# Kernel tuning notes

Measured on AMD Instinct MI355X. Metric: run time of the kernel, lower is better.

Reference implementation:

```python
import jax, jax.numpy as jnp
import numpy as np

DIM = 512
H = 8
HD = DIM // H
B = 1
S = 4096
SCALE = HD ** -0.5


def setup_inputs() -> dict:
    key = jax.random.key(0)
    k1, k2, k3, k4, k5 = jax.random.split(key, 5)
    bound = DIM ** -0.5
    x = jax.random.normal(k1, (B, S, DIM), dtype=jnp.float32)
    q_param = jax.random.uniform(k2, (DIM, H, HD), dtype=jnp.float32, minval=-bound, maxval=bound)
    k_param = jax.random.uniform(k3, (DIM, H, HD), dtype=jnp.float32, minval=-bound, maxval=bound)
    v_param = jax.random.uniform(k4, (DIM, H, HD), dtype=jnp.float32, minval=-bound, maxval=bound)
    p_param = jax.random.uniform(k5, (H, HD, DIM), dtype=jnp.float32, minval=-bound, maxval=bound)
    return {"x": x, "q_param": q_param, "k_param": k_param, "v_param": v_param, "p_param": p_param}


def reference(x, q_param, k_param, v_param, p_param):
    q = jnp.einsum('bsc,chd->bshd', x, q_param) * SCALE
    k = jnp.einsum('btc,chd->bthd', x, k_param)
    v = jnp.einsum('btc,chd->bthd', x, v_param)
    attn = jax.nn.softmax(jnp.einsum('bshd,bthd->bhst', q, k), axis=-1)  # [B,H,S,S]
    o = jnp.einsum('bhst,bthd->bshd', attn, v)
    return jnp.einsum('bshd,hdc->bsc', o, p_param)
```

## Files before the change

kernel.cpp:

```cpp
#include <hip/hip_runtime.h>
#include <hip/hip_bf16.h>
#include <stdint.h>

#define S_LEN 4096
#define DIM   512
#define NH    8
#define HD    64
#define QSCALE 0.18033688011112042f

typedef __attribute__((ext_vector_type(8))) short short8;
typedef __attribute__((ext_vector_type(4))) float f32x4;
typedef __attribute__((ext_vector_type(16))) float f32x16;
typedef __attribute__((ext_vector_type(2))) unsigned uint2v;

__device__ __forceinline__ uint32_t pk2(float lo, float hi) {
  union { __hip_bfloat162 h; uint32_t u; } cv;
  cv.h = __float22bfloat162_rn(float2{lo, hi});
  return cv.u;
}
__device__ __forceinline__ ushort bf1(float x) {
  union { __hip_bfloat16 b; ushort u; } cv;
  cv.b = __float2bfloat16(x);
  return cv.u;
}
__device__ __forceinline__ float bf2f(ushort u) {
  union { uint32_t u; float f; } cv;
  cv.u = (uint32_t)u << 16;
  return cv.f;
}
__device__ __forceinline__ float fexp2(float x) {
  float r;
  asm("v_exp_f32 %0, %1" : "=v"(r) : "v"(x));
  return r;
}

__global__ __launch_bounds__(256)
void cast_x(const float* __restrict__ src, ushort* __restrict__ dst) {
  const int i = (blockIdx.x * 256 + threadIdx.x) * 8;
  const float4 a = *reinterpret_cast<const float4*>(src + i);
  const float4 b = *reinterpret_cast<const float4*>(src + i + 4);
  uint4 o;
  o.x = pk2(a.x, a.y); o.y = pk2(a.z, a.w);
  o.z = pk2(b.x, b.y); o.w = pk2(b.z, b.w);
  *reinterpret_cast<uint4*>(dst + i) = o;
}

__global__ __launch_bounds__(256)
void transpose_w(const float* __restrict__ qp, const float* __restrict__ kp,
                 const float* __restrict__ vp, const float* __restrict__ pp,
                 ushort* __restrict__ wbT, ushort* __restrict__ ppT) {
  __shared__ float L[64][65];
  const int z = blockIdx.z;
  const float* src = (z == 0) ? qp : (z == 1) ? kp : (z == 2) ? vp : pp;
  ushort* dst = (z < 3) ? (wbT + (size_t)z * 512 * 512) : ppT;
  const float scale = (z == 0) ? QSCALE : 1.0f;
  const int k0 = blockIdx.x * 64, n0 = blockIdx.y * 64;
  const int r = threadIdx.x >> 2, c0 = (threadIdx.x & 3) * 16;

#pragma unroll
  for (int j = 0; j < 4; ++j) {
    const float4 v =
        *reinterpret_cast<const float4*>(&src[(k0 + r) * 512 + n0 + c0 + 4 * j]);
    L[r][c0 + 4 * j + 0] = v.x * scale;
    L[r][c0 + 4 * j + 1] = v.y * scale;
    L[r][c0 + 4 * j + 2] = v.z * scale;
    L[r][c0 + 4 * j + 3] = v.w * scale;
  }
  __syncthreads();

  uint4 u0, u1;
  u0.x = pk2(L[c0 + 0][r], L[c0 + 1][r]);
  u0.y = pk2(L[c0 + 2][r], L[c0 + 3][r]);
  u0.z = pk2(L[c0 + 4][r], L[c0 + 5][r]);
  u0.w = pk2(L[c0 + 6][r], L[c0 + 7][r]);
  u1.x = pk2(L[c0 + 8][r], L[c0 + 9][r]);
  u1.y = pk2(L[c0 + 10][r], L[c0 + 11][r]);
  u1.z = pk2(L[c0 + 12][r], L[c0 + 13][r]);
  u1.w = pk2(L[c0 + 14][r], L[c0 + 15][r]);
  ushort* d = dst + (size_t)(n0 + r) * 512 + k0 + c0;
  *reinterpret_cast<uint4*>(d) = u0;
  *reinterpret_cast<uint4*>(d + 8) = u1;
}

template <int MODE>
__global__ __launch_bounds__(256)
void gemm_bf16(const ushort* __restrict__ A, const ushort* __restrict__ Bt,
               void* __restrict__ Cout) {
  __shared__ __align__(16) unsigned char lds[24576];
  const int tid = threadIdx.x;
  const int m0 = blockIdx.x * 128, n0 = blockIdx.y * 64;
  const int lane = tid & 63, w = tid >> 6;
  const int wm = w >> 1, wn = w & 1;
  const int q = lane & 15, g = lane >> 4;
  f32x4 acc[4][2] = {};

  const int ar = tid >> 1, ah = tid & 1;
  const int br = tid >> 2, bq = tid & 3;

  for (int k0 = 0; k0 < 512; k0 += 64) {
    const ushort* ag = A + (size_t)(m0 + ar) * 512 + k0 + ah * 32;
    const uint4 a0 = *reinterpret_cast<const uint4*>(ag);
    const uint4 a1 = *reinterpret_cast<const uint4*>(ag + 8);
    const uint4 a2 = *reinterpret_cast<const uint4*>(ag + 16);
    const uint4 a3 = *reinterpret_cast<const uint4*>(ag + 24);
    const ushort* bg = Bt + (size_t)(n0 + br) * 512 + k0 + bq * 16;
    const uint4 b0 = *reinterpret_cast<const uint4*>(bg);
    const uint4 b1 = *reinterpret_cast<const uint4*>(bg + 8);
    __syncthreads();
    {
      unsigned char* ab = lds + ar * 128;
      const int asw = (ar & 7) << 4;
      *reinterpret_cast<uint4*>(ab + ((ah * 64 + 0) ^ asw)) = a0;
      *reinterpret_cast<uint4*>(ab + ((ah * 64 + 16) ^ asw)) = a1;
      *reinterpret_cast<uint4*>(ab + ((ah * 64 + 32) ^ asw)) = a2;
      *reinterpret_cast<uint4*>(ab + ((ah * 64 + 48) ^ asw)) = a3;
      unsigned char* bb = lds + 16384 + br * 128;
      const int bsw = (br & 7) << 4;
      *reinterpret_cast<uint4*>(bb + ((bq * 32 + 0) ^ bsw)) = b0;
      *reinterpret_cast<uint4*>(bb + ((bq * 32 + 16) ^ bsw)) = b1;
    }
    __syncthreads();

#pragma unroll
    for (int ks = 0; ks < 2; ++ks) {
      short8 bf[2];
#pragma unroll
      for (int ni = 0; ni < 2; ++ni) {
        const int rn = wn * 32 + ni * 16 + q;
        bf[ni] = *reinterpret_cast<const short8*>(
            lds + 16384 + rn * 128 + ((64 * ks + 16 * g) ^ ((rn & 7) << 4)));
      }
#pragma unroll
      for (int mi = 0; mi < 4; ++mi) {
        const int rm = wm * 64 + mi * 16 + q;
        const short8 af = *reinterpret_cast<const short8*>(
            lds + rm * 128 + ((64 * ks + 16 * g) ^ ((rm & 7) << 4)));
#pragma unroll
        for (int ni = 0; ni < 2; ++ni)
          acc[mi][ni] = __builtin_amdgcn_mfma_f32_16x16x32_bf16(
              af, bf[ni], acc[mi][ni], 0, 0, 0);
      }
    }
  }

  if (MODE == 0) {
    ushort* C = (ushort*)Cout;
    const int which = n0 >> 9;
#pragma unroll
    for (int ni = 0; ni < 2; ++ni) {
      const int n = n0 + wn * 32 + ni * 16 + q;
      const int rem = n & 511, hh = rem >> 6, d = rem & 63;
      if (which == 2) {
        ushort* base = C + (size_t)(2 * NH + hh) * (size_t)(S_LEN * HD) +
                       (size_t)d * S_LEN;
#pragma unroll
        for (int mi = 0; mi < 4; ++mi) {
          const int s = m0 + wm * 64 + mi * 16 + 4 * g;
          uint2 pw;
          pw.x = pk2(acc[mi][ni][0], acc[mi][ni][1]);
          pw.y = pk2(acc[mi][ni][2], acc[mi][ni][3]);
          *reinterpret_cast<uint2*>(base + s) = pw;
        }
      } else {
        ushort* base =
            C + ((size_t)which * NH + hh) * (size_t)(S_LEN * HD) + d;
#pragma unroll
        for (int mi = 0; mi < 4; ++mi) {
          const int s = m0 + wm * 64 + mi * 16 + 4 * g;
#pragma unroll
          for (int r = 0; r < 4; ++r)
            base[(size_t)(s + r) * HD] = bf1(acc[mi][ni][r]);
        }
      }
    }
  } else {
    float* C = (float*)Cout;
#pragma unroll
    for (int ni = 0; ni < 2; ++ni) {
      const int n = n0 + wn * 32 + ni * 16 + q;
#pragma unroll
      for (int mi = 0; mi < 4; ++mi) {
        const int s = m0 + wm * 64 + mi * 16 + 4 * g;
#pragma unroll
        for (int r = 0; r < 4; ++r)
          C[(size_t)(s + r) * 512 + n] = acc[mi][ni][r];
      }
    }
  }
}

__global__ __launch_bounds__(256, 4)
void attn_mfma32(const ushort* __restrict__ QKV, ushort* __restrict__ Opart,
                 float2* __restrict__ ML) {
  __shared__ __align__(16) unsigned char lds[32768];
  const int tid = threadIdx.x;
  const int combo = blockIdx.x;
  const int h = combo & 7, z = combo >> 3;
  const int qb = blockIdx.y;
  const int lane = tid & 63, w = tid >> 6;
  const int r31 = lane & 31, hh = lane >> 5;

  const size_t plane = (size_t)S_LEN * HD;
  const ushort* Qp = QKV + (size_t)h * plane;
  const ushort* Kp = QKV + (size_t)(NH + h) * plane;
  const ushort* Vp = QKV + (size_t)(2 * NH + h) * plane;

  const int qrow = qb * 128 + w * 32 + r31;

  short8 qf[4];
  {
    const ushort* qptr = Qp + (size_t)qrow * HD + 8 * hh;
#pragma unroll
    for (int ks = 0; ks < 4; ++ks)
      qf[ks] = *reinterpret_cast<const short8*>(qptr + 16 * ks);
  }

  int raddr[4];
#pragma unroll
  for (int ks = 0; ks < 4; ++ks)
    raddr[ks] = r31 * 128 + (((2 * ks + hh) ^ (r31 & 7)) << 4);

  const int trow = tid >> 2, seg = tid & 3;
  const int swr = (trow & 7) << 4;
  const int wk0 = trow * 128 + ((seg * 32) ^ swr);
  const int wk1 = trow * 128 + ((seg * 32 + 16) ^ swr);
  const ushort* kgbase = Kp + (size_t)(z * 1024 + trow) * HD + seg * 16;
  const ushort* vgbase = Vp + (size_t)trow * S_LEN + z * 1024 + seg * 16;

  f32x16 o[2] = {};
  float m_i = -1e30f, l_i = 0.f;

  uint4 kA = *reinterpret_cast<const uint4*>(kgbase);
  uint4 kB = *reinterpret_cast<const uint4*>(kgbase + 8);
  uint4 vA = *reinterpret_cast<const uint4*>(vgbase);
  uint4 vB = *reinterpret_cast<const uint4*>(vgbase + 8);

  for (int t = 0; t < 16; ++t) {
    const int po = (t & 1) << 14;
    *reinterpret_cast<uint4*>(lds + (wk0 | po)) = kA;
    *reinterpret_cast<uint4*>(lds + (wk1 | po)) = kB;
    *reinterpret_cast<uint4*>(lds + ((8192 + wk0) | po)) = vA;
    *reinterpret_cast<uint4*>(lds + ((8192 + wk1) | po)) = vB;
    __syncthreads();

    const int tn = (t + 1) & 15;
    kA = *reinterpret_cast<const uint4*>(kgbase + tn * 4096);
    kB = *reinterpret_cast<const uint4*>(kgbase + tn * 4096 + 8);
    vA = *reinterpret_cast<const uint4*>(vgbase + tn * 64);
    vB = *reinterpret_cast<const uint4*>(vgbase + tn * 64 + 8);

    f32x16 s0 = {}, s1 = {};
#pragma unroll
    for (int ks = 0; ks < 4; ++ks) {
      const short8 a0 =
          *reinterpret_cast<const short8*>(lds + (raddr[ks] | po));
      const short8 a1 =
          *reinterpret_cast<const short8*>(lds + ((raddr[ks] + 4096) | po));
      s0 = __builtin_amdgcn_mfma_f32_32x32x16_bf16(a0, qf[ks], s0, 0, 0, 0);
      s1 = __builtin_amdgcn_mfma_f32_32x32x16_bf16(a1, qf[ks], s1, 0, 0, 0);
    }

    float mv[8];
#pragma unroll
    for (int i = 0; i < 8; ++i)
      mv[i] = fmaxf(fmaxf(s0[i], s0[i + 8]), fmaxf(s1[i], s1[i + 8]));
#pragma unroll
    for (int i = 0; i < 4; ++i) mv[i] = fmaxf(mv[i], mv[i + 4]);
    float mx = fmaxf(fmaxf(mv[0], mv[1]), fmaxf(mv[2], mv[3]));
    mx = fmaxf(mx, __shfl_xor(mx, 32));

    const bool grow = mx > m_i + 8.0f;
    if (__any(grow)) {
      const float mn = grow ? mx : m_i;
      const float alpha = grow ? fexp2(m_i - mn) : 1.0f;
      l_i *= alpha;
#pragma unroll
      for (int i = 0; i < 16; ++i) { o[0][i] *= alpha; o[1][i] *= alpha; }
      m_i = mn;
    }

    float r0 = 0.f, r1 = 0.f, r2 = 0.f, r3 = 0.f;
#pragma unroll
    for (int i = 0; i < 16; i += 4) {
      s0[i + 0] = fexp2(s0[i + 0] - m_i); r0 += s0[i + 0];
      s0[i + 1] = fexp2(s0[i + 1] - m_i); r1 += s0[i + 1];
      s0[i + 2] = fexp2(s0[i + 2] - m_i); r2 += s0[i + 2];
      s0[i + 3] = fexp2(s0[i + 3] - m_i); r3 += s0[i + 3];
      s1[i + 0] = fexp2(s1[i + 0] - m_i); r0 += s1[i + 0];
      s1[i + 1] = fexp2(s1[i + 1] - m_i); r1 += s1[i + 1];
      s1[i + 2] = fexp2(s1[i + 2] - m_i); r2 += s1[i + 2];
      s1[i + 3] = fexp2(s1[i + 3] - m_i); r3 += s1[i + 3];
    }
    float rs = (r0 + r1) + (r2 + r3);
    rs += __shfl_xor(rs, 32);
    l_i += rs;

    short8 pf[4];
#pragma unroll
    for (int ks = 0; ks < 4; ++ks) {
      const int bb = 2 * (ks & 1);
      float p0, p1, p2, p3, p4, p5, p6, p7;
      if (ks < 2) {
        p0 = s0[4 * bb + 0]; p1 = s0[4 * bb + 1]; p2 = s0[4 * bb + 2];
        p3 = s0[4 * bb + 3]; p4 = s0[4 * bb + 4]; p5 = s0[4 * bb + 5];
        p6 = s0[4 * bb + 6]; p7 = s0[4 * bb + 7];
      } else {
        p0 = s1[4 * bb + 0]; p1 = s1[4 * bb + 1]; p2 = s1[4 * bb + 2];
        p3 = s1[4 * bb + 3]; p4 = s1[4 * bb + 4]; p5 = s1[4 * bb + 5];
        p6 = s1[4 * bb + 6]; p7 = s1[4 * bb + 7];
      }
      const uint32_t u00 = pk2(p0, p1), u01 = pk2(p2, p3);
      const uint32_t u10 = pk2(p4, p5), u11 = pk2(p6, p7);
      const uint2v se0 = __builtin_amdgcn_permlane32_swap(u00, u10, false, false);
      const uint2v se1 = __builtin_amdgcn_permlane32_swap(u01, u11, false, false);
      uint32_t fr[4] = {se0.x, se1.x, se0.y, se1.y};
      pf[ks] = *reinterpret_cast<short8*>(fr);
    }

#pragma unroll
    for (int dt = 0; dt < 2; ++dt)
#pragma unroll
      for (int ks = 0; ks < 4; ++ks) {
        const short8 vf = *reinterpret_cast<const short8*>(
            lds + ((8192 + dt * 4096 + raddr[ks]) | po));
        o[dt] = __builtin_amdgcn_mfma_f32_32x32x16_bf16(vf, pf[ks], o[dt],
                                                        0, 0, 0);
      }
  }

  if (lane < 32) ML[(size_t)combo * S_LEN + qrow] = float2{m_i, l_i};
  ushort* ob = Opart + (size_t)combo * 64 * S_LEN + qrow;
#pragma unroll
  for (int dt = 0; dt < 2; ++dt)
#pragma unroll
    for (int r = 0; r < 16; ++r) {
      const int d = 32 * dt + (r & 3) + 8 * (r >> 2) + 4 * hh;
      ob[(size_t)d * S_LEN] = bf1(o[dt][r]);
    }
}

__global__ __launch_bounds__(256)
void combine(const ushort* __restrict__ Opart, const float2* __restrict__ ML,
             ushort* __restrict__ ob) {
  const int t = threadIdx.x;
  const int qq = t & 63, ds = t >> 6;
  const int q = blockIdx.x * 64 + qq;
  const int h = blockIdx.y;

  float m = -1e30f, mz[4], lz[4];
#pragma unroll
  for (int z = 0; z < 4; ++z) {
    const float2 v = ML[(size_t)(z * 8 + h) * S_LEN + q];
    mz[z] = v.x; lz[z] = v.y;
    m = fmaxf(m, v.x);
  }
  float wz[4], l = 0.f;
#pragma unroll
  for (int z = 0; z < 4; ++z) {
    wz[z] = fexp2(mz[z] - m);
    l += wz[z] * lz[z];
  }
  const float inv = 1.0f / l;

  float acc[16];
#pragma unroll
  for (int i = 0; i < 16; ++i) acc[i] = 0.f;
#pragma unroll
  for (int z = 0; z < 4; ++z) {
    const ushort* src =
        Opart + ((size_t)(z * 8 + h) * 64 + ds * 16) * S_LEN + q;
#pragma unroll
    for (int i = 0; i < 16; ++i)
      acc[i] += wz[z] * bf2f(src[(size_t)i * S_LEN]);
  }
  uint32_t pk[8];
#pragma unroll
  for (int i = 0; i < 8; ++i)
    pk[i] = pk2(acc[2 * i] * inv, acc[2 * i + 1] * inv);
  ushort* dst = ob + (size_t)q * DIM + h * 64 + ds * 16;
  *reinterpret_cast<uint4*>(dst) = *reinterpret_cast<uint4*>(pk);
  *reinterpret_cast<uint4*>(dst + 8) = *reinterpret_cast<uint4*>(pk + 4);
}

extern "C" void kernel_launch(void* const* d_in, const int* in_sizes, int n_in,
                              void* d_out, int out_size, void* d_ws, size_t ws_size,
                              hipStream_t stream) {
  const float* x  = (const float*)d_in[0];
  const float* qp = (const float*)d_in[1];
  const float* kp = (const float*)d_in[2];
  const float* vp = (const float*)d_in[3];
  const float* pp = (const float*)d_in[4];
  float* out = (float*)d_out;

  unsigned char* ws = (unsigned char*)d_ws;
  ushort* xb    = (ushort*)(ws);
  ushort* qkvb  = (ushort*)(ws + ((size_t)4 << 20));
  ushort* ob    = (ushort*)(ws + ((size_t)16 << 20));
  ushort* wbT   = (ushort*)(ws + ((size_t)20 << 20));
  ushort* ppT   = (ushort*)(ws + ((size_t)22 << 20));
  ushort* opart = (ushort*)(ws + ((size_t)23 << 20));
  float2* ml    = (float2*)(ws + ((size_t)39 << 20));

  cast_x<<<dim3(1024), dim3(256), 0, stream>>>(x, xb);
  transpose_w<<<dim3(8, 8, 4), dim3(256), 0, stream>>>(qp, kp, vp, pp, wbT, ppT);
  gemm_bf16<0><<<dim3(32, 24), dim3(256), 0, stream>>>(xb, wbT, qkvb);
  attn_mfma32<<<dim3(32, 32), dim3(256), 0, stream>>>(qkvb, opart, ml);
  combine<<<dim3(64, 8), dim3(256), 0, stream>>>(opart, ml, ob);
  gemm_bf16<1><<<dim3(32, 8), dim3(256), 0, stream>>>(ob, ppT, out);
}
```

Before: 96.71 us.

## Widen GEMM tiles, double attention block size, store partials row-major

The projection GEMMs now use 128x128 tiles instead of 128x64, which halves the grid and raises reuse of each A tile. The attention kernel runs 512 threads per block (8 waves covering 256 query rows) and shares each K/V tile load across twice as many waves. Attention partial outputs are written row-major with packed 8-byte stores, so the combine kernel can read them with vector loads instead of strided scalar loads, and the normalization is folded into the weights. Risks: fewer GEMM blocks for the small N=512 output GEMM, higher register pressure with 16 accumulators, and lower occupancy for the larger attention blocks.

```diff
diff --git a/kernel.cpp b/kernel.cpp
--- a/kernel.cpp
+++ b/kernel.cpp
@@ -83,19 +83,18 @@
 }
 
 template <int MODE>
-__global__ __launch_bounds__(256)
+__global__ __launch_bounds__(256, 2)
 void gemm_bf16(const ushort* __restrict__ A, const ushort* __restrict__ Bt,
                void* __restrict__ Cout) {
-  __shared__ __align__(16) unsigned char lds[24576];
+  __shared__ __align__(16) unsigned char lds[32768];
   const int tid = threadIdx.x;
-  const int m0 = blockIdx.x * 128, n0 = blockIdx.y * 64;
+  const int m0 = blockIdx.x * 128, n0 = blockIdx.y * 128;
   const int lane = tid & 63, w = tid >> 6;
   const int wm = w >> 1, wn = w & 1;
   const int q = lane & 15, g = lane >> 4;
-  f32x4 acc[4][2] = {};
+  f32x4 acc[4][4] = {};
 
   const int ar = tid >> 1, ah = tid & 1;
-  const int br = tid >> 2, bq = tid & 3;
 
   for (int k0 = 0; k0 < 512; k0 += 64) {
     const ushort* ag = A + (size_t)(m0 + ar) * 512 + k0 + ah * 32;
@@ -103,30 +102,33 @@
     const uint4 a1 = *reinterpret_cast<const uint4*>(ag + 8);
     const uint4 a2 = *reinterpret_cast<const uint4*>(ag + 16);
     const uint4 a3 = *reinterpret_cast<const uint4*>(ag + 24);
-    const ushort* bg = Bt + (size_t)(n0 + br) * 512 + k0 + bq * 16;
+    const ushort* bg = Bt + (size_t)(n0 + ar) * 512 + k0 + ah * 32;
     const uint4 b0 = *reinterpret_cast<const uint4*>(bg);
     const uint4 b1 = *reinterpret_cast<const uint4*>(bg + 8);
+    const uint4 b2 = *reinterpret_cast<const uint4*>(bg + 16);
+    const uint4 b3 = *reinterpret_cast<const uint4*>(bg + 24);
     __syncthreads();
     {
+      const int asw = (ar & 7) << 4;
       unsigned char* ab = lds + ar * 128;
-      const int asw = (ar & 7) << 4;
       *reinterpret_cast<uint4*>(ab + ((ah * 64 + 0) ^ asw)) = a0;
       *reinterpret_cast<uint4*>(ab + ((ah * 64 + 16) ^ asw)) = a1;
       *reinterpret_cast<uint4*>(ab + ((ah * 64 + 32) ^ asw)) = a2;
       *reinterpret_cast<uint4*>(ab + ((ah * 64 + 48) ^ asw)) = a3;
-      unsigned char* bb = lds + 16384 + br * 128;
-      const int bsw = (br & 7) << 4;
-      *reinterpret_cast<uint4*>(bb + ((bq * 32 + 0) ^ bsw)) = b0;
-      *reinterpret_cast<uint4*>(bb + ((bq * 32 + 16) ^ bsw)) = b1;
+      unsigned char* bb = lds + 16384 + ar * 128;
+      *reinterpret_cast<uint4*>(bb + ((ah * 64 + 0) ^ asw)) = b0;
+      *reinterpret_cast<uint4*>(bb + ((ah * 64 + 16) ^ asw)) = b1;
+      *reinterpret_cast<uint4*>(bb + ((ah * 64 + 32) ^ asw)) = b2;
+      *reinterpret_cast<uint4*>(bb + ((ah * 64 + 48) ^ asw)) = b3;
     }
     __syncthreads();
 
 #pragma unroll
     for (int ks = 0; ks < 2; ++ks) {
-      short8 bf[2];
-#pragma unroll
-      for (int ni = 0; ni < 2; ++ni) {
-        const int rn = wn * 32 + ni * 16 + q;
+      short8 bf[4];
+#pragma unroll
+      for (int ni = 0; ni < 4; ++ni) {
+        const int rn = wn * 64 + ni * 16 + q;
         bf[ni] = *reinterpret_cast<const short8*>(
             lds + 16384 + rn * 128 + ((64 * ks + 16 * g) ^ ((rn & 7) << 4)));
       }
@@ -136,7 +138,7 @@
         const short8 af = *reinterpret_cast<const short8*>(
             lds + rm * 128 + ((64 * ks + 16 * g) ^ ((rm & 7) << 4)));
 #pragma unroll
-        for (int ni = 0; ni < 2; ++ni)
+        for (int ni = 0; ni < 4; ++ni)
           acc[mi][ni] = __builtin_amdgcn_mfma_f32_16x16x32_bf16(
               af, bf[ni], acc[mi][ni], 0, 0, 0);
       }
@@ -147,8 +149,8 @@
     ushort* C = (ushort*)Cout;
     const int which = n0 >> 9;
 #pragma unroll
-    for (int ni = 0; ni < 2; ++ni) {
-      const int n = n0 + wn * 32 + ni * 16 + q;
+    for (int ni = 0; ni < 4; ++ni) {
+      const int n = n0 + wn * 64 + ni * 16 + q;
       const int rem = n & 511, hh = rem >> 6, d = rem & 63;
       if (which == 2) {
         ushort* base = C + (size_t)(2 * NH + hh) * (size_t)(S_LEN * HD) +
@@ -176,8 +178,8 @@
   } else {
     float* C = (float*)Cout;
 #pragma unroll
-    for (int ni = 0; ni < 2; ++ni) {
-      const int n = n0 + wn * 32 + ni * 16 + q;
+    for (int ni = 0; ni < 4; ++ni) {
+      const int n = n0 + wn * 64 + ni * 16 + q;
 #pragma unroll
       for (int mi = 0; mi < 4; ++mi) {
         const int s = m0 + wm * 64 + mi * 16 + 4 * g;
@@ -189,7 +191,7 @@
   }
 }
 
-__global__ __launch_bounds__(256, 4)
+__global__ __launch_bounds__(512, 4)
 void attn_mfma32(const ushort* __restrict__ QKV, ushort* __restrict__ Opart,
                  float2* __restrict__ ML) {
   __shared__ __align__(16) unsigned char lds[32768];
@@ -205,7 +207,7 @@
   const ushort* Kp = QKV + (size_t)(NH + h) * plane;
   const ushort* Vp = QKV + (size_t)(2 * NH + h) * plane;
 
-  const int qrow = qb * 128 + w * 32 + r31;
+  const int qrow = qb * 256 + w * 32 + r31;
 
   short8 qf[4];
   {
@@ -220,34 +222,26 @@
   for (int ks = 0; ks < 4; ++ks)
     raddr[ks] = r31 * 128 + (((2 * ks + hh) ^ (r31 & 7)) << 4);
 
-  const int trow = tid >> 2, seg = tid & 3;
-  const int swr = (trow & 7) << 4;
-  const int wk0 = trow * 128 + ((seg * 32) ^ swr);
-  const int wk1 = trow * 128 + ((seg * 32 + 16) ^ swr);
-  const ushort* kgbase = Kp + (size_t)(z * 1024 + trow) * HD + seg * 16;
-  const ushort* vgbase = Vp + (size_t)trow * S_LEN + z * 1024 + seg * 16;
+  const int trow = tid >> 3, seg = tid & 7;
+  const int wk = trow * 128 + ((seg * 16) ^ ((trow & 7) << 4));
+  const ushort* kgbase = Kp + (size_t)(z * 1024 + trow) * HD + seg * 8;
+  const ushort* vgbase = Vp + (size_t)trow * S_LEN + z * 1024 + seg * 8;
 
   f32x16 o[2] = {};
   float m_i = -1e30f, l_i = 0.f;
 
   uint4 kA = *reinterpret_cast<const uint4*>(kgbase);
-  uint4 kB = *reinterpret_cast<const uint4*>(kgbase + 8);
   uint4 vA = *reinterpret_cast<const uint4*>(vgbase);
-  uint4 vB = *reinterpret_cast<const uint4*>(vgbase + 8);
 
   for (int t = 0; t < 16; ++t) {
     const int po = (t & 1) << 14;
-    *reinterpret_cast<uint4*>(lds + (wk0 | po)) = kA;
-    *reinterpret_cast<uint4*>(lds + (wk1 | po)) = kB;
-    *reinterpret_cast<uint4*>(lds + ((8192 + wk0) | po)) = vA;
-    *reinterpret_cast<uint4*>(lds + ((8192 + wk1) | po)) = vB;
+    *reinterpret_cast<uint4*>(lds + (wk | po)) = kA;
+    *reinterpret_cast<uint4*>(lds + ((8192 + wk) | po)) = vA;
     __syncthreads();
 
     const int tn = (t + 1) & 15;
     kA = *reinterpret_cast<const uint4*>(kgbase + tn * 4096);
-    kB = *reinterpret_cast<const uint4*>(kgbase + tn * 4096 + 8);
     vA = *reinterpret_cast<const uint4*>(vgbase + tn * 64);
-    vB = *reinterpret_cast<const uint4*>(vgbase + tn * 64 + 8);
 
     f32x16 s0 = {}, s1 = {};
 #pragma unroll
@@ -329,13 +323,16 @@
   }
 
   if (lane < 32) ML[(size_t)combo * S_LEN + qrow] = float2{m_i, l_i};
-  ushort* ob = Opart + (size_t)combo * 64 * S_LEN + qrow;
+  ushort* ob = Opart + ((size_t)combo * S_LEN + qrow) * HD;
 #pragma unroll
   for (int dt = 0; dt < 2; ++dt)
 #pragma unroll
-    for (int r = 0; r < 16; ++r) {
-      const int d = 32 * dt + (r & 3) + 8 * (r >> 2) + 4 * hh;
-      ob[(size_t)d * S_LEN] = bf1(o[dt][r]);
+    for (int rq = 0; rq < 4; ++rq) {
+      const int d = 32 * dt + 8 * rq + 4 * hh;
+      uint2 pw;
+      pw.x = pk2(o[dt][4 * rq + 0], o[dt][4 * rq + 1]);
+      pw.y = pk2(o[dt][4 * rq + 2], o[dt][4 * rq + 3]);
+      *reinterpret_cast<uint2*>(ob + d) = pw;
     }
 }
 
@@ -361,6 +358,8 @@
     l += wz[z] * lz[z];
   }
   const float inv = 1.0f / l;
+#pragma unroll
+  for (int z = 0; z < 4; ++z) wz[z] *= inv;
 
   float acc[16];
 #pragma unroll
@@ -368,15 +367,21 @@
 #pragma unroll
   for (int z = 0; z < 4; ++z) {
     const ushort* src =
-        Opart + ((size_t)(z * 8 + h) * 64 + ds * 16) * S_LEN + q;
-#pragma unroll
-    for (int i = 0; i < 16; ++i)
-      acc[i] += wz[z] * bf2f(src[(size_t)i * S_LEN]);
+        Opart + (((size_t)(z * 8 + h) * S_LEN) + q) * HD + ds * 16;
+    const uint4 u0 = *reinterpret_cast<const uint4*>(src);
+    const uint4 u1 = *reinterpret_cast<const uint4*>(src + 8);
+    const ushort* e0 = reinterpret_cast<const ushort*>(&u0);
+    const ushort* e1 = reinterpret_cast<const ushort*>(&u1);
+#pragma unroll
+    for (int i = 0; i < 8; ++i) {
+      acc[i] = fmaf(wz[z], bf2f(e0[i]), acc[i]);
+      acc[i + 8] = fmaf(wz[z], bf2f(e1[i]), acc[i + 8]);
+    }
   }
   uint32_t pk[8];
 #pragma unroll
   for (int i = 0; i < 8; ++i)
-    pk[i] = pk2(acc[2 * i] * inv, acc[2 * i + 1] * inv);
+    pk[i] = pk2(acc[2 * i], acc[2 * i + 1]);
   ushort* dst = ob + (size_t)q * DIM + h * 64 + ds * 16;
   *reinterpret_cast<uint4*>(dst) = *reinterpret_cast<uint4*>(pk);
   *reinterpret_cast<uint4*>(dst + 8) = *reinterpret_cast<uint4*>(pk + 4);
@@ -403,8 +408,8 @@
 
   cast_x<<<dim3(1024), dim3(256), 0, stream>>>(x, xb);
   transpose_w<<<dim3(8, 8, 4), dim3(256), 0, stream>>>(qp, kp, vp, pp, wbT, ppT);
-  gemm_bf16<0><<<dim3(32, 24), dim3(256), 0, stream>>>(xb, wbT, qkvb);
-  attn_mfma32<<<dim3(32, 32), dim3(256), 0, stream>>>(qkvb, opart, ml);
+  gemm_bf16<0><<<dim3(32, 12), dim3(256), 0, stream>>>(xb, wbT, qkvb);
+  attn_mfma32<<<dim3(32, 16), dim3(512), 0, stream>>>(qkvb, opart, ml);
   combine<<<dim3(64, 8), dim3(256), 0, stream>>>(opart, ml, ob);
-  gemm_bf16<1><<<dim3(32, 8), dim3(256), 0, stream>>>(ob, ppT, out);
-}
+  gemm_bf16<1><<<dim3(32, 4), dim3(256), 0, stream>>>(ob, ppT, out);
+}
```

Result: slower. 98.69 us (+2.1%).
